# Optimization experiments

Measured on AMD Instinct MI355X. Metric: run time of the kernel, lower is better.

Reference implementation:

```python
import jax, jax.numpy as jnp
import numpy as np
import math

D_MODEL = 512
NHEAD = 8
HEAD = D_MODEL // NHEAD


def _pe(length, d):
    pos = np.arange(length)[:, None].astype(np.float32)
    div = np.exp(np.arange(0, d, 2).astype(np.float32) * (-math.log(10000.0) / d))
    pe = np.zeros((length, d), np.float32)
    pe[:, 0::2] = np.sin(pos * div)
    pe[:, 1::2] = np.cos(pos * div)
    return jnp.asarray(pe)


def _ln(x, g, b, eps=1e-5):
    m = x.mean(-1, keepdims=True)
    v = ((x - m) ** 2).mean(-1, keepdims=True)
    return (x - m) / jnp.sqrt(v + eps) * g + b


def _mha(q_in, k_in, v_in, w_in, b_in, w_out, b_out, mask=None):
    d = q_in.shape[-1]
    wq, wk, wv = jnp.split(w_in, 3, axis=0)
    bq, bk, bv = jnp.split(b_in, 3, axis=0)
    B, Sq, _ = q_in.shape
    Sk = k_in.shape[1]
    q = (q_in @ wq.T + bq).reshape(B, Sq, NHEAD, HEAD)
    k = (k_in @ wk.T + bk).reshape(B, Sk, NHEAD, HEAD)
    v = (v_in @ wv.T + bv).reshape(B, Sk, NHEAD, HEAD)
    s = jnp.einsum('bqhd,bkhd->bhqk', q, k) / math.sqrt(HEAD)
    if mask is not None:
        s = s + mask
    a = jax.nn.softmax(s, axis=-1)
    o = jnp.einsum('bhqk,bkhd->bqhd', a, v).reshape(B, Sq, d)
    return o @ w_out.T + b_out


def setup_inputs() -> dict:
    rng = np.random.default_rng(0)
    def r(*s):
        return jnp.asarray(rng.standard_normal(s, dtype=np.float32) * 0.02)
    L, d, ff, di, do = 6, 512, 2048, 64, 64
    B, S, T = 4, 512, 256
    return dict(
        src=jnp.asarray(rng.standard_normal((B, S, di), dtype=np.float32)),
        tgt=jnp.asarray(rng.standard_normal((B, T, do), dtype=np.float32)),
        enc_in_w=r(d, di), enc_in_b=r(d),
        dec_in_w=r(d, do), dec_in_b=r(d),
        out_w=r(do, d), out_b=r(do),
        enc_attn_w=r(L, 3 * d, d), enc_attn_b=r(L, 3 * d),
        enc_out_w=r(L, d, d), enc_out_b=r(L, d),
        enc_ff1_w=r(L, ff, d), enc_ff1_b=r(L, ff),
        enc_ff2_w=r(L, d, ff), enc_ff2_b=r(L, d),
        enc_ln1_g=jnp.ones((L, d)), enc_ln1_b=jnp.zeros((L, d)),
        enc_ln2_g=jnp.ones((L, d)), enc_ln2_b=jnp.zeros((L, d)),
        dec_sa_w=r(L, 3 * d, d), dec_sa_b=r(L, 3 * d),
        dec_sa_out_w=r(L, d, d), dec_sa_out_b=r(L, d),
        dec_ca_w=r(L, 3 * d, d), dec_ca_b=r(L, 3 * d),
        dec_ca_out_w=r(L, d, d), dec_ca_out_b=r(L, d),
        dec_ff1_w=r(L, ff, d), dec_ff1_b=r(L, ff),
        dec_ff2_w=r(L, d, ff), dec_ff2_b=r(L, d),
        dec_ln1_g=jnp.ones((L, d)), dec_ln1_b=jnp.zeros((L, d)),
        dec_ln2_g=jnp.ones((L, d)), dec_ln2_b=jnp.zeros((L, d)),
        dec_ln3_g=jnp.ones((L, d)), dec_ln3_b=jnp.zeros((L, d)),
    )


def reference(src, tgt, enc_in_w, enc_in_b, dec_in_w, dec_in_b, out_w, out_b,
              enc_attn_w, enc_attn_b, enc_out_w, enc_out_b,
              enc_ff1_w, enc_ff1_b, enc_ff2_w, enc_ff2_b,
              enc_ln1_g, enc_ln1_b, enc_ln2_g, enc_ln2_b,
              dec_sa_w, dec_sa_b, dec_sa_out_w, dec_sa_out_b,
              dec_ca_w, dec_ca_b, dec_ca_out_w, dec_ca_out_b,
              dec_ff1_w, dec_ff1_b, dec_ff2_w, dec_ff2_b,
              dec_ln1_g, dec_ln1_b, dec_ln2_g, dec_ln2_b, dec_ln3_g, dec_ln3_b):
    d = D_MODEL
    sq = math.sqrt(d)
    S, T = src.shape[1], tgt.shape[1]
    L = enc_attn_w.shape[0]
    # encoder: 'cosine' pos encoding (dropout disabled / eval)
    x = (src @ enc_in_w.T + enc_in_b) * sq + _pe(S, d)[None]
    for i in range(L):
        a = _mha(x, x, x, enc_attn_w[i], enc_attn_b[i], enc_out_w[i], enc_out_b[i])
        x = _ln(x + a, enc_ln1_g[i], enc_ln1_b[i])
        f = jax.nn.relu(x @ enc_ff1_w[i].T + enc_ff1_b[i]) @ enc_ff2_w[i].T + enc_ff2_b[i]
        x = _ln(x + f, enc_ln2_g[i], enc_ln2_b[i])
    memory = x
    # decoder: teacher-forced prefix loop == single causal-masked pass.
    # NOTE: original adds pe[0] to EVERY step (pos_encoder on a length-1 slice).
    y = (tgt @ dec_in_w.T + dec_in_b) * sq + _pe(1, d)[0]
    mask = jnp.where(jnp.tril(jnp.ones((T, T), bool)), 0.0, -1e9).astype(y.dtype)
    for i in range(L):
        a = _mha(y, y, y, dec_sa_w[i], dec_sa_b[i], dec_sa_out_w[i], dec_sa_out_b[i], mask)
        y = _ln(y + a, dec_ln1_g[i], dec_ln1_b[i])
        c = _mha(y, memory, memory, dec_ca_w[i], dec_ca_b[i], dec_ca_out_w[i], dec_ca_out_b[i])
        y = _ln(y + c, dec_ln2_g[i], dec_ln2_b[i])
        f = jax.nn.relu(y @ dec_ff1_w[i].T + dec_ff1_b[i]) @ dec_ff2_w[i].T + dec_ff2_b[i]
        y = _ln(y + f, dec_ln3_g[i], dec_ln3_b[i])
    return y @ out_w.T + out_b
```

## Files before the change

kernel.cpp:

```cpp
#include <hip/hip_runtime.h>
#include <hip/hip_bf16.h>
#include <math.h>

#define BB 4
#define SEQ 512
#define TGT 256
#define DM 512
#define FFD 2048
#define NH 8
#define HD 64
#define NL 6

typedef unsigned short u16;
typedef __attribute__((ext_vector_type(2))) unsigned short us2;
typedef __attribute__((ext_vector_type(4))) float f4;
typedef __attribute__((ext_vector_type(4))) unsigned short us4;
typedef __attribute__((ext_vector_type(8))) unsigned short us8;
typedef __attribute__((ext_vector_type(8))) short s8;

__device__ inline u16 f2b(float f) {
    __hip_bfloat16 h = __float2bfloat16(f);
    return *reinterpret_cast<u16*>(&h);
}
__device__ inline float b2f(u16 u) {
    unsigned int x = ((unsigned int)u) << 16;
    float f;
    __builtin_memcpy(&f, &x, 4);
    return f;
}
__device__ inline us4 cvt4(f4 v) {
    us4 u;
    u.x = f2b(v.x); u.y = f2b(v.y); u.z = f2b(v.z); u.w = f2b(v.w);
    return u;
}

struct CastSegs {
    const float* src[24];
    u16* dst[24];
    int cum[25];
    int nseg;
};

__global__ __launch_bounds__(256) void castseg_k(CastSegs cs)
{
    const int g0 = blockIdx.x << 11;
    int s = 0;
    while (g0 >= cs.cum[s + 1]) s++;
    const f4* __restrict__ sp = (const f4*)cs.src[s];
    us4* __restrict__ dp = (us4*)cs.dst[s];
    const int base = g0 - cs.cum[s] + (int)threadIdx.x;

    f4 v[8];
#pragma unroll
    for (int k = 0; k < 8; k++) v[k] = sp[base + (k << 8)];
#pragma unroll
    for (int k = 0; k < 8; k++) dp[base + (k << 8)] = cvt4(v[k]);
}

__global__ void kvbias_k(const float* __restrict__ dec_ca_b, float* __restrict__ out)
{
    int idx = blockIdx.x * blockDim.x + threadIdx.x;
    if (idx >= NL * 2 * DM) return;
    int layer = idx >> 10, j = idx & 1023;
    out[idx] = dec_ca_b[layer * 3 * DM + DM + j];
}

template <int RELU, int OUTF32, int BM, int PE>
__global__ __launch_bounds__(256) void mgemm_k(
    const u16* __restrict__ A, const u16* __restrict__ W,
    const float* __restrict__ bias, const u16* __restrict__ resid,
    void* __restrict__ Cv, int M, int N, int K, float alpha)
{
    constexpr int MI = BM / 32;
    __shared__ u16 As[2][BM][72];
    __shared__ u16 Bs[2][64][72];
    const int bm = blockIdx.y * BM, bn = blockIdx.x * 64;
    const int tid = threadIdx.x;
    const int wave = tid >> 6, lane = tid & 63;
    const int wr = (wave >> 1) * (BM / 2), wc = (wave & 1) * 32;
    const int lm = lane & 15, quad = lane >> 4;
    const int sbr = tid >> 2, sbc = (tid & 3) * 16;
    const int sar = (BM == 64) ? (tid >> 2) : (tid >> 3);
    const int sac = (BM == 64) ? ((tid & 3) * 16) : ((tid & 7) * 8);

    const u16* Arow = A + (size_t)(bm + sar) * K + sac;
    const u16* Wrow = W + (size_t)(bn + sbr) * K + sbc;

    us8 a0 = *(const us8*)(Arow);
    us8 a1;
    if (BM == 64) a1 = *(const us8*)(Arow + 8);
    us8 b0 = *(const us8*)(Wrow);
    us8 b1 = *(const us8*)(Wrow + 8);

    f4 acc[MI][2];
#pragma unroll
    for (int i = 0; i < MI; i++)
#pragma unroll
        for (int j = 0; j < 2; j++) acc[i][j] = (f4)(0.f);

    const int nk = K >> 6;
    *(us8*)&As[0][sar][sac] = a0;
    if (BM == 64) *(us8*)&As[0][sar][sac + 8] = a1;
    *(us8*)&Bs[0][sbr][sbc] = b0;
    *(us8*)&Bs[0][sbr][sbc + 8] = b1;
    __syncthreads();

    for (int t = 0; t < nk; t++) {
        const int cb = t & 1;
        if (t + 1 < nk) {
            int off = (t + 1) << 6;
            a0 = *(const us8*)(Arow + off);
            if (BM == 64) a1 = *(const us8*)(Arow + off + 8);
            b0 = *(const us8*)(Wrow + off);
            b1 = *(const us8*)(Wrow + off + 8);
        }
#pragma unroll
        for (int ks = 0; ks < 2; ks++) {
            s8 af[MI], bfr[2];
#pragma unroll
            for (int i = 0; i < MI; i++) af[i] = *(const s8*)&As[cb][wr + i * 16 + lm][ks * 32 + quad * 8];
#pragma unroll
            for (int j = 0; j < 2; j++) bfr[j] = *(const s8*)&Bs[cb][wc + j * 16 + lm][ks * 32 + quad * 8];
#pragma unroll
            for (int i = 0; i < MI; i++)
#pragma unroll
                for (int j = 0; j < 2; j++)
                    acc[i][j] = __builtin_amdgcn_mfma_f32_16x16x32_bf16(af[i], bfr[j], acc[i][j], 0, 0, 0);
        }
        if (t + 1 < nk) {
            const int nb = cb ^ 1;
            *(us8*)&As[nb][sar][sac] = a0;
            if (BM == 64) *(us8*)&As[nb][sar][sac + 8] = a1;
            *(us8*)&Bs[nb][sbr][sbc] = b0;
            *(us8*)&Bs[nb][sbr][sbc + 8] = b1;
            __syncthreads();
        }
    }

#pragma unroll
    for (int j = 0; j < 2; j++) {
        int n = bn + wc + j * 16 + lm;
        float bv = bias[n];
        float dv = 0.f;
        if (PE == 1) dv = expf((float)(n & ~1) * (-9.210340371976184f / (float)DM));
#pragma unroll
        for (int i = 0; i < MI; i++) {
#pragma unroll
            for (int r = 0; r < 4; r++) {
                int m = bm + wr + i * 16 + quad * 4 + r;
                float v = (acc[i][j][r] + bv) * alpha;
                if (PE == 1) {
                    float ang = (float)(m & (SEQ - 1)) * dv;
                    v += (n & 1) ? cosf(ang) : sinf(ang);
                }
                if (PE == 2) { if (n & 1) v += 1.f; }
                if (RELU) v = fmaxf(v, 0.f);
                size_t off = (size_t)m * N + n;
                if (resid) v += b2f(resid[off]);
                if (OUTF32) ((float*)Cv)[off] = v;
                else        ((u16*)Cv)[off]  = f2b(v);
            }
        }
    }
}

template <int RELU, int KVMAP>
__global__ __launch_bounds__(256) void mgemm128_k(
    const u16* __restrict__ A, const u16* __restrict__ W,
    const float* __restrict__ bias, u16* __restrict__ C,
    int M, int N, int K)
{
    __shared__ u16 As[2][64][72];
    __shared__ u16 Bs[2][128][72];
    const int bm = blockIdx.y * 64, bn = blockIdx.x * 128;
    const int tid = threadIdx.x;
    const int wave = tid >> 6, lane = tid & 63;
    const int wr = (wave >> 1) * 32, wc = (wave & 1) * 64;
    const int lm = lane & 15, quad = lane >> 4;
    const int sar = tid >> 2, sac = (tid & 3) * 16;
    const int sbr = tid >> 1, sbc = (tid & 1) * 32;

    int brow = bn + sbr;
    if (KVMAP) brow = (brow >> 10) * (3 * DM) + DM + (brow & 1023);

    const u16* Arow = A + (size_t)(bm + sar) * K + sac;
    const u16* Wrow = W + (size_t)brow * K + sbc;

    us8 a0 = *(const us8*)(Arow);
    us8 a1 = *(const us8*)(Arow + 8);
    us8 b0 = *(const us8*)(Wrow);
    us8 b1 = *(const us8*)(Wrow + 8);
    us8 b2 = *(const us8*)(Wrow + 16);
    us8 b3 = *(const us8*)(Wrow + 24);

    f4 acc[2][4];
#pragma unroll
    for (int i = 0; i < 2; i++)
#pragma unroll
        for (int j = 0; j < 4; j++) acc[i][j] = (f4)(0.f);

    const int nk = K >> 6;
    *(us8*)&As[0][sar][sac]     = a0;
    *(us8*)&As[0][sar][sac + 8] = a1;
    *(us8*)&Bs[0][sbr][sbc]      = b0;
    *(us8*)&Bs[0][sbr][sbc + 8]  = b1;
    *(us8*)&Bs[0][sbr][sbc + 16] = b2;
    *(us8*)&Bs[0][sbr][sbc + 24] = b3;
    __syncthreads();

    for (int t = 0; t < nk; t++) {
        const int cb = t & 1;
        if (t + 1 < nk) {
            int off = (t + 1) << 6;
            a0 = *(const us8*)(Arow + off);
            a1 = *(const us8*)(Arow + off + 8);
            b0 = *(const us8*)(Wrow + off);
            b1 = *(const us8*)(Wrow + off + 8);
            b2 = *(const us8*)(Wrow + off + 16);
            b3 = *(const us8*)(Wrow + off + 24);
        }
#pragma unroll
        for (int ks = 0; ks < 2; ks++) {
            s8 af[2], bfr[4];
#pragma unroll
            for (int i = 0; i < 2; i++) af[i] = *(const s8*)&As[cb][wr + i * 16 + lm][ks * 32 + quad * 8];
#pragma unroll
            for (int j = 0; j < 4; j++) bfr[j] = *(const s8*)&Bs[cb][wc + j * 16 + lm][ks * 32 + quad * 8];
#pragma unroll
            for (int i = 0; i < 2; i++)
#pragma unroll
                for (int j = 0; j < 4; j++)
                    acc[i][j] = __builtin_amdgcn_mfma_f32_16x16x32_bf16(af[i], bfr[j], acc[i][j], 0, 0, 0);
        }
        if (t + 1 < nk) {
            const int nb = cb ^ 1;
            *(us8*)&As[nb][sar][sac]     = a0;
            *(us8*)&As[nb][sar][sac + 8] = a1;
            *(us8*)&Bs[nb][sbr][sbc]      = b0;
            *(us8*)&Bs[nb][sbr][sbc + 8]  = b1;
            *(us8*)&Bs[nb][sbr][sbc + 16] = b2;
            *(us8*)&Bs[nb][sbr][sbc + 24] = b3;
            __syncthreads();
        }
    }

#pragma unroll
    for (int j = 0; j < 4; j++) {
        int n = bn + wc + j * 16 + lm;
        float bv = bias[n];
#pragma unroll
        for (int i = 0; i < 2; i++) {
#pragma unroll
            for (int r = 0; r < 4; r++) {
                int m = bm + wr + i * 16 + quad * 4 + r;
                float v = acc[i][j][r] + bv;
                if (RELU) v = fmaxf(v, 0.f);
                C[(size_t)m * N + n] = f2b(v);
            }
        }
    }
}

template <int CAUSAL>
__global__ __launch_bounds__(256) void flash_k(
    const u16* __restrict__ Q, int qs,
    const u16* __restrict__ Kp, int ks,
    const u16* __restrict__ V, int vs,
    u16* __restrict__ O, int Sq, int Sk)
{
    __shared__ u16 Qs[64][72];
    __shared__ u16 Ks[128][72];
    __shared__ u16 Vs[64][136];
    __shared__ u16 Ps[4][16][136];
    const int bm = blockIdx.x * 64;
    const int bh = blockIdx.y, b = bh >> 3, h = bh & 7;
    const int tid = threadIdx.x;
    const int wave = tid >> 6, lane = tid & 63;
    const int lm = lane & 15, quad = lane >> 4;

    const u16* Qb = Q + (size_t)(b * Sq + bm) * qs + h * HD;
    {
        int r = tid >> 2, c = (tid & 3) * 16;
        *(us8*)&Qs[r][c]     = *(const us8*)(Qb + (size_t)r * qs + c);
        *(us8*)&Qs[r][c + 8] = *(const us8*)(Qb + (size_t)r * qs + c + 8);
    }

    float mrow[4], lrow[4];
    f4 o[4];
#pragma unroll
    for (int r = 0; r < 4; r++) { mrow[r] = -1e30f; lrow[r] = 0.f; }
#pragma unroll
    for (int nt = 0; nt < 4; nt++) o[nt] = (f4)(0.f);

    const u16* Kb = Kp + (size_t)(b * Sk) * ks + h * HD;
    const u16* Vb = V + (size_t)(b * Sk) * vs + h * HD;
    int nkt = Sk >> 7;
    if (CAUSAL) { int lim = (bm + 63) / 128 + 1; if (lim < nkt) nkt = lim; }

    const int kr = tid >> 3, kc8 = (tid & 7) * 8;
    const int vr = tid & 127, vh = (tid >> 7) * 32;

    for (int kt = 0; kt < nkt; kt++) {
        const u16* Kt = Kb + ((size_t)kt << 7) * ks;
        const u16* Vt = Vb + ((size_t)kt << 7) * vs;
#pragma unroll
        for (int p = 0; p < 4; p++) {
            int r = p * 32 + kr;
            *(us8*)&Ks[r][kc8] = *(const us8*)(Kt + (size_t)r * ks + kc8);
        }
        {
            us8 vv[4];
#pragma unroll
            for (int j = 0; j < 4; j++)
                vv[j] = *(const us8*)(Vt + (size_t)vr * vs + vh + j * 8);
#pragma unroll
            for (int j = 0; j < 4; j++)
#pragma unroll
                for (int e = 0; e < 8; e++)
                    Vs[vh + j * 8 + e][vr] = vv[j][e];
        }
        __syncthreads();

        f4 sa[8];
#pragma unroll
        for (int nt = 0; nt < 8; nt++) sa[nt] = (f4)(0.f);
#pragma unroll
        for (int ks2 = 0; ks2 < 2; ks2++) {
            s8 aq = *(const s8*)&Qs[wave * 16 + lm][ks2 * 32 + quad * 8];
#pragma unroll
            for (int nt = 0; nt < 8; nt++) {
                s8 bk = *(const s8*)&Ks[nt * 16 + lm][ks2 * 32 + quad * 8];
                sa[nt] = __builtin_amdgcn_mfma_f32_16x16x32_bf16(aq, bk, sa[nt], 0, 0, 0);
            }
        }
        float tmx[4] = {-1e30f, -1e30f, -1e30f, -1e30f};
#pragma unroll
        for (int nt = 0; nt < 8; nt++) {
#pragma unroll
            for (int r = 0; r < 4; r++) {
                float v = sa[nt][r] * 0.125f;
                if (CAUSAL) {
                    int col = (kt << 7) + nt * 16 + lm;
                    int row = bm + wave * 16 + quad * 4 + r;
                    if (col > row) v = -1e30f;
                }
                sa[nt][r] = v;
                tmx[r] = fmaxf(tmx[r], v);
            }
        }
#pragma unroll
        for (int st = 1; st < 16; st <<= 1)
#pragma unroll
            for (int r = 0; r < 4; r++) tmx[r] = fmaxf(tmx[r], __shfl_xor(tmx[r], st));
        float al[4];
#pragma unroll
        for (int r = 0; r < 4; r++) {
            float mn = fmaxf(mrow[r], tmx[r]);
            al[r] = __expf(mrow[r] - mn);
            mrow[r] = mn;
        }
        float ts[4] = {0.f, 0.f, 0.f, 0.f};
#pragma unroll
        for (int nt = 0; nt < 8; nt++) {
#pragma unroll
            for (int r = 0; r < 4; r++) {
                float pe = __expf(sa[nt][r] - mrow[r]);
                sa[nt][r] = pe;
                ts[r] += pe;
            }
        }
#pragma unroll
        for (int st = 1; st < 16; st <<= 1)
#pragma unroll
            for (int r = 0; r < 4; r++) ts[r] += __shfl_xor(ts[r], st);
#pragma unroll
        for (int r = 0; r < 4; r++) lrow[r] = lrow[r] * al[r] + ts[r];
#pragma unroll
        for (int nt = 0; nt < 4; nt++)
#pragma unroll
            for (int r = 0; r < 4; r++) o[nt][r] *= al[r];
#pragma unroll
        for (int nt = 0; nt < 8; nt++)
#pragma unroll
            for (int r = 0; r < 4; r++)
                Ps[wave][quad * 4 + r][nt * 16 + lm] = f2b(sa[nt][r]);
#pragma unroll
        for (int kc = 0; kc < 4; kc++) {
            s8 ap = *(const s8*)&Ps[wave][lm][kc * 32 + quad * 8];
#pragma unroll
            for (int nt = 0; nt < 4; nt++) {
                s8 bv = *(const s8*)&Vs[nt * 16 + lm][kc * 32 + quad * 8];
                o[nt] = __builtin_amdgcn_mfma_f32_16x16x32_bf16(ap, bv, o[nt], 0, 0, 0);
            }
        }
        __syncthreads();
    }

    float inv[4];
#pragma unroll
    for (int r = 0; r < 4; r++) inv[r] = 1.f / lrow[r];
#pragma unroll
    for (int nt = 0; nt < 4; nt++) {
#pragma unroll
        for (int r = 0; r < 4; r++) {
            int m = bm + wave * 16 + quad * 4 + r;
            O[(size_t)(b * Sq + m) * DM + h * HD + nt * 16 + lm] = f2b(o[nt][r] * inv[r]);
        }
    }
}

__global__ __launch_bounds__(256) void ln_k(u16* __restrict__ x,
                                            const float* __restrict__ g,
                                            const float* __restrict__ b)
{
    const int wave = threadIdx.x >> 6, lane = threadIdx.x & 63;
    const int row = blockIdx.x * 4 + wave;
    u16* xr = x + (size_t)row * DM + lane * 8;
    us8 v8 = *(const us8*)xr;
    float v[8];
    float s = 0.f;
#pragma unroll
    for (int e = 0; e < 8; e++) { v[e] = b2f(v8[e]); s += v[e]; }
#pragma unroll
    for (int st = 1; st < 64; st <<= 1) s += __shfl_xor(s, st);
    float mean = s * (1.f / DM);
    float q = 0.f;
#pragma unroll
    for (int e = 0; e < 8; e++) { float d = v[e] - mean; q += d * d; }
#pragma unroll
    for (int st = 1; st < 64; st <<= 1) q += __shfl_xor(q, st);
    float rstd = rsqrtf(q * (1.f / DM) + 1e-5f);
    f4 g0 = *(const f4*)(g + lane * 8), g1 = *(const f4*)(g + lane * 8 + 4);
    f4 b0 = *(const f4*)(b + lane * 8), b1 = *(const f4*)(b + lane * 8 + 4);
    us8 o;
#pragma unroll
    for (int e = 0; e < 4; e++) {
        o[e]     = f2b((v[e]     - mean) * rstd * g0[e] + b0[e]);
        o[e + 4] = f2b((v[e + 4] - mean) * rstd * g1[e] + b1[e]);
    }
    *(us8*)xr = o;
}

static inline dim3 mg64(int M, int N) { return dim3(N / 64, M / 64); }
static inline dim3 mg32(int M, int N) { return dim3(N / 64, M / 32); }
static inline dim3 mg128(int M, int N) { return dim3(N / 128, M / 64); }

extern "C" void kernel_launch(void* const* d_in, const int* in_sizes, int n_in,
                              void* d_out, int out_size, void* d_ws, size_t ws_size,
                              hipStream_t stream)
{
    const float* src       = (const float*)d_in[0];
    const float* tgt       = (const float*)d_in[1];
    const float* enc_in_w  = (const float*)d_in[2];
    const float* enc_in_b  = (const float*)d_in[3];
    const float* dec_in_w  = (const float*)d_in[4];
    const float* dec_in_b  = (const float*)d_in[5];
    const float* out_w     = (const float*)d_in[6];
    const float* out_b     = (const float*)d_in[7];
    const float* enc_attn_w = (const float*)d_in[8];
    const float* enc_attn_b = (const float*)d_in[9];
    const float* enc_out_w  = (const float*)d_in[10];
    const float* enc_out_b  = (const float*)d_in[11];
    const float* enc_ff1_w  = (const float*)d_in[12];
    const float* enc_ff1_b  = (const float*)d_in[13];
    const float* enc_ff2_w  = (const float*)d_in[14];
    const float* enc_ff2_b  = (const float*)d_in[15];
    const float* enc_ln1_g  = (const float*)d_in[16];
    const float* enc_ln1_b  = (const float*)d_in[17];
    const float* enc_ln2_g  = (const float*)d_in[18];
    const float* enc_ln2_b  = (const float*)d_in[19];
    const float* dec_sa_w     = (const float*)d_in[20];
    const float* dec_sa_b     = (const float*)d_in[21];
    const float* dec_sa_out_w = (const float*)d_in[22];
    const float* dec_sa_out_b = (const float*)d_in[23];
    const float* dec_ca_w     = (const float*)d_in[24];
    const float* dec_ca_b     = (const float*)d_in[25];
    const float* dec_ca_out_w = (const float*)d_in[26];
    const float* dec_ca_out_b = (const float*)d_in[27];
    const float* dec_ff1_w    = (const float*)d_in[28];
    const float* dec_ff1_b    = (const float*)d_in[29];
    const float* dec_ff2_w    = (const float*)d_in[30];
    const float* dec_ff2_b    = (const float*)d_in[31];
    const float* dec_ln1_g    = (const float*)d_in[32];
    const float* dec_ln1_b    = (const float*)d_in[33];
    const float* dec_ln2_g    = (const float*)d_in[34];
    const float* dec_ln2_b    = (const float*)d_in[35];
    const float* dec_ln3_g    = (const float*)d_in[36];
    const float* dec_ln3_b    = (const float*)d_in[37];

    const int ME = BB * SEQ;
    const int MD = BB * TGT;
    const int BH = BB * NH;
    const float SQD = 22.627416997969522f;

    const size_t SZ_ATTN = (size_t)NL * 3 * DM * DM;
    const size_t SZ_OUT  = (size_t)NL * DM * DM;
    const size_t SZ_FF   = (size_t)NL * FFD * DM;

    float* fp = (float*)d_ws;
    float* kvbias = fp; fp += NL * 2 * DM;
    u16* p = (u16*)fp;
    u16* xa   = p; p += (size_t)ME * DM;
    u16* xb   = p; p += (size_t)ME * DM;
    u16* reg1 = p; p += (size_t)ME * FFD;
    u16* tbuf = p; p += (size_t)ME * DM;
    u16* ya   = p; p += (size_t)MD * DM;
    u16* yb   = p; p += (size_t)MD * DM;
    u16* kvall = p; p += (size_t)ME * NL * 2 * DM;
    u16* src_b     = p; p += (size_t)ME * HD;
    u16* tgt_b     = p; p += (size_t)MD * HD;
    u16* enc_in_wb = p; p += (size_t)DM * HD;
    u16* dec_in_wb = p; p += (size_t)DM * HD;
    u16* out_wb    = p; p += (size_t)HD * DM;
    u16* enc_at_wb = p; p += SZ_ATTN;
    u16* enc_ow_wb = p; p += SZ_OUT;
    u16* enc_f1_wb = p; p += SZ_FF;
    u16* enc_f2_wb = p; p += SZ_FF;
    u16* dec_sa_wb = p; p += SZ_ATTN;
    u16* dec_sao_wb = p; p += SZ_OUT;
    u16* dec_ca_wb = p; p += SZ_ATTN;
    u16* dec_cao_wb = p; p += SZ_OUT;
    u16* dec_f1_wb = p; p += SZ_FF;
    u16* dec_f2_wb = p; p += SZ_FF;

    CastSegs cs;
    int ns = 0;
    auto seg = [&](const float* s, u16* d, size_t n) {
        cs.src[ns] = s; cs.dst[ns] = d;
        cs.cum[ns + 1] = cs.cum[ns] + (int)(n / 4);
        ns++;
    };
    cs.cum[0] = 0;
    seg(src,          src_b,     (size_t)ME * HD);
    seg(tgt,          tgt_b,     (size_t)MD * HD);
    seg(enc_in_w,     enc_in_wb, (size_t)DM * HD);
    seg(dec_in_w,     dec_in_wb, (size_t)DM * HD);
    seg(out_w,        out_wb,    (size_t)HD * DM);
    seg(enc_attn_w,   enc_at_wb, SZ_ATTN);
    seg(enc_out_w,    enc_ow_wb, SZ_OUT);
    seg(enc_ff1_w,    enc_f1_wb, SZ_FF);
    seg(enc_ff2_w,    enc_f2_wb, SZ_FF);
    seg(dec_sa_w,     dec_sa_wb, SZ_ATTN);
    seg(dec_sa_out_w, dec_sao_wb, SZ_OUT);
    seg(dec_ca_w,     dec_ca_wb, SZ_ATTN);
    seg(dec_ca_out_w, dec_cao_wb, SZ_OUT);
    seg(dec_ff1_w,    dec_f1_wb, SZ_FF);
    seg(dec_ff2_w,    dec_f2_wb, SZ_FF);
    cs.nseg = ns;
    castseg_k<<<cs.cum[ns] >> 11, 256, 0, stream>>>(cs);
    kvbias_k<<<(NL * 2 * DM + 255) / 256, 256, 0, stream>>>(dec_ca_b, kvbias);

    mgemm_k<0, 0, 64, 1><<<mg64(ME, DM), 256, 0, stream>>>(src_b, enc_in_wb, enc_in_b, nullptr, xa, ME, DM, HD, SQD);

    u16* cur = xa; u16* alt = xb;
    for (int i = 0; i < NL; i++) {
        const u16* W = enc_at_wb + (size_t)i * 3 * DM * DM;
        const float* Bw = enc_attn_b + (size_t)i * 3 * DM;
        mgemm128_k<0, 0><<<mg128(ME, 3 * DM), 256, 0, stream>>>(cur, W, Bw, reg1, ME, 3 * DM, DM);
        flash_k<0><<<dim3(SEQ / 64, BH), 256, 0, stream>>>(reg1, 3 * DM, reg1 + DM, 3 * DM, reg1 + 2 * DM, 3 * DM, tbuf, SEQ, SEQ);
        mgemm_k<0, 0, 32, 0><<<mg32(ME, DM), 256, 0, stream>>>(tbuf, enc_ow_wb + (size_t)i * DM * DM, enc_out_b + (size_t)i * DM, cur, alt, ME, DM, DM, 1.f);
        ln_k<<<ME / 4, 256, 0, stream>>>(alt, enc_ln1_g + (size_t)i * DM, enc_ln1_b + (size_t)i * DM);
        { u16* t = cur; cur = alt; alt = t; }
        mgemm128_k<1, 0><<<mg128(ME, FFD), 256, 0, stream>>>(cur, enc_f1_wb + (size_t)i * FFD * DM, enc_ff1_b + (size_t)i * FFD, reg1, ME, FFD, DM);
        mgemm_k<0, 0, 32, 0><<<mg32(ME, DM), 256, 0, stream>>>(reg1, enc_f2_wb + (size_t)i * DM * FFD, enc_ff2_b + (size_t)i * DM, cur, alt, ME, DM, FFD, 1.f);
        ln_k<<<ME / 4, 256, 0, stream>>>(alt, enc_ln2_g + (size_t)i * DM, enc_ln2_b + (size_t)i * DM);
        { u16* t = cur; cur = alt; alt = t; }
    }
    u16* mem = cur;

    mgemm128_k<0, 1><<<mg128(ME, NL * 2 * DM), 256, 0, stream>>>(mem, dec_ca_wb, kvbias, kvall, ME, NL * 2 * DM, DM);

    mgemm_k<0, 0, 32, 2><<<mg32(MD, DM), 256, 0, stream>>>(tgt_b, dec_in_wb, dec_in_b, nullptr, ya, MD, DM, HD, SQD);

    u16* dc = ya; u16* da = yb;
    for (int i = 0; i < NL; i++) {
        const u16* W = dec_sa_wb + (size_t)i * 3 * DM * DM;
        const float* Bw = dec_sa_b + (size_t)i * 3 * DM;
        mgemm128_k<0, 0><<<mg128(MD, 3 * DM), 256, 0, stream>>>(dc, W, Bw, reg1, MD, 3 * DM, DM);
        flash_k<1><<<dim3(TGT / 64, BH), 256, 0, stream>>>(reg1, 3 * DM, reg1 + DM, 3 * DM, reg1 + 2 * DM, 3 * DM, tbuf, TGT, TGT);
        mgemm_k<0, 0, 32, 0><<<mg32(MD, DM), 256, 0, stream>>>(tbuf, dec_sao_wb + (size_t)i * DM * DM, dec_sa_out_b + (size_t)i * DM, dc, da, MD, DM, DM, 1.f);
        ln_k<<<MD / 4, 256, 0, stream>>>(da, dec_ln1_g + (size_t)i * DM, dec_ln1_b + (size_t)i * DM);
        { u16* t = dc; dc = da; da = t; }

        const u16* Wc = dec_ca_wb + (size_t)i * 3 * DM * DM;
        const float* Bc = dec_ca_b + (size_t)i * 3 * DM;
        u16* qbuf = reg1;
        mgemm_k<0, 0, 32, 0><<<mg32(MD, DM), 256, 0, stream>>>(dc, Wc, Bc, nullptr, qbuf, MD, DM, DM, 1.f);
        const u16* kvl = kvall + (size_t)i * 2 * DM;
        flash_k<0><<<dim3(TGT / 64, BH), 256, 0, stream>>>(qbuf, DM, kvl, NL * 2 * DM, kvl + DM, NL * 2 * DM, tbuf, TGT, SEQ);
        mgemm_k<0, 0, 32, 0><<<mg32(MD, DM), 256, 0, stream>>>(tbuf, dec_cao_wb + (size_t)i * DM * DM, dec_ca_out_b + (size_t)i * DM, dc, da, MD, DM, DM, 1.f);
        ln_k<<<MD / 4, 256, 0, stream>>>(da, dec_ln2_g + (size_t)i * DM, dec_ln2_b + (size_t)i * DM);
        { u16* t = dc; dc = da; da = t; }

        mgemm128_k<1, 0><<<mg128(MD, FFD), 256, 0, stream>>>(dc, dec_f1_wb + (size_t)i * FFD * DM, dec_ff1_b + (size_t)i * FFD, reg1, MD, FFD, DM);
        mgemm_k<0, 0, 32, 0><<<mg32(MD, DM), 256, 0, stream>>>(reg1, dec_f2_wb + (size_t)i * DM * FFD, dec_ff2_b + (size_t)i * DM, dc, da, MD, DM, FFD, 1.f);
        ln_k<<<MD / 4, 256, 0, stream>>>(da, dec_ln3_g + (size_t)i * DM, dec_ln3_b + (size_t)i * DM);
        { u16* t = dc; dc = da; da = t; }
    }

    mgemm_k<0, 1, 32, 0><<<mg32(MD, HD), 256, 0, stream>>>(dc, out_wb, out_b, nullptr, (float*)d_out, MD, HD, DM, 1.f);
}
```

Measured before the change: 1.273 ms.

## Drop upfront weight cast; load fp32 weights and convert inside GEMM tile loads

Removes the large upfront fp32-to-bf16 conversion pass over all layer weights. The GEMM kernels instead read fp32 weights directly and convert them while staging tiles into shared memory. This avoids a separate full write and reread of the weights, at the cost of twice the global bytes per weight tile inside each GEMM plus the conversion work there. The flash kernel's V transpose load also changes from vectorized row reads to scalar per-element loads.

```diff
diff --git a/kernel.cpp b/kernel.cpp
--- a/kernel.cpp
+++ b/kernel.cpp
@@ -12,7 +12,6 @@
 #define NL 6
 
 typedef unsigned short u16;
-typedef __attribute__((ext_vector_type(2))) unsigned short us2;
 typedef __attribute__((ext_vector_type(4))) float f4;
 typedef __attribute__((ext_vector_type(4))) unsigned short us4;
 typedef __attribute__((ext_vector_type(8))) unsigned short us8;
@@ -34,10 +33,30 @@
     return u;
 }
 
+template <int WF32> struct wvec {};
+template <> struct wvec<0> { us8 v; };
+template <> struct wvec<1> { f4 lo, hi; };
+
+__device__ inline void wload(wvec<0>& d, const void* W, size_t idx) {
+    d.v = *(const us8*)((const u16*)W + idx);
+}
+__device__ inline void wload(wvec<1>& d, const void* W, size_t idx) {
+    const float* p = (const float*)W + idx;
+    d.lo = *(const f4*)p; d.hi = *(const f4*)(p + 4);
+}
+__device__ inline us8 wcvt(const wvec<0>& d) { return d.v; }
+__device__ inline us8 wcvt(const wvec<1>& d) {
+    us4 l = cvt4(d.lo), h = cvt4(d.hi);
+    us8 o;
+#pragma unroll
+    for (int e = 0; e < 4; e++) { o[e] = l[e]; o[e + 4] = h[e]; }
+    return o;
+}
+
 struct CastSegs {
-    const float* src[24];
-    u16* dst[24];
-    int cum[25];
+    const float* src[8];
+    u16* dst[8];
+    int cum[9];
     int nseg;
 };
 
@@ -65,9 +84,9 @@
     out[idx] = dec_ca_b[layer * 3 * DM + DM + j];
 }
 
-template <int RELU, int OUTF32, int BM, int PE>
+template <int RELU, int OUTF32, int BM, int PE, int WF32>
 __global__ __launch_bounds__(256) void mgemm_k(
-    const u16* __restrict__ A, const u16* __restrict__ W,
+    const u16* __restrict__ A, const void* __restrict__ W,
     const float* __restrict__ bias, const u16* __restrict__ resid,
     void* __restrict__ Cv, int M, int N, int K, float alpha)
 {
@@ -84,13 +103,14 @@
     const int sac = (BM == 64) ? ((tid & 3) * 16) : ((tid & 7) * 8);
 
     const u16* Arow = A + (size_t)(bm + sar) * K + sac;
-    const u16* Wrow = W + (size_t)(bn + sbr) * K + sbc;
+    const size_t wb0 = (size_t)(bn + sbr) * K + sbc;
 
     us8 a0 = *(const us8*)(Arow);
     us8 a1;
     if (BM == 64) a1 = *(const us8*)(Arow + 8);
-    us8 b0 = *(const us8*)(Wrow);
-    us8 b1 = *(const us8*)(Wrow + 8);
+    wvec<WF32> b0, b1;
+    wload(b0, W, wb0);
+    wload(b1, W, wb0 + 8);
 
     f4 acc[MI][2];
 #pragma unroll
@@ -101,8 +121,8 @@
     const int nk = K >> 6;
     *(us8*)&As[0][sar][sac] = a0;
     if (BM == 64) *(us8*)&As[0][sar][sac + 8] = a1;
-    *(us8*)&Bs[0][sbr][sbc] = b0;
-    *(us8*)&Bs[0][sbr][sbc + 8] = b1;
+    *(us8*)&Bs[0][sbr][sbc] = wcvt(b0);
+    *(us8*)&Bs[0][sbr][sbc + 8] = wcvt(b1);
     __syncthreads();
 
     for (int t = 0; t < nk; t++) {
@@ -111,8 +131,8 @@
             int off = (t + 1) << 6;
             a0 = *(const us8*)(Arow + off);
             if (BM == 64) a1 = *(const us8*)(Arow + off + 8);
-            b0 = *(const us8*)(Wrow + off);
-            b1 = *(const us8*)(Wrow + off + 8);
+            wload(b0, W, wb0 + off);
+            wload(b1, W, wb0 + off + 8);
         }
 #pragma unroll
         for (int ks = 0; ks < 2; ks++) {
@@ -131,8 +151,8 @@
             const int nb = cb ^ 1;
             *(us8*)&As[nb][sar][sac] = a0;
             if (BM == 64) *(us8*)&As[nb][sar][sac + 8] = a1;
-            *(us8*)&Bs[nb][sbr][sbc] = b0;
-            *(us8*)&Bs[nb][sbr][sbc + 8] = b1;
+            *(us8*)&Bs[nb][sbr][sbc] = wcvt(b0);
+            *(us8*)&Bs[nb][sbr][sbc + 8] = wcvt(b1);
             __syncthreads();
         }
     }
@@ -164,9 +184,9 @@
     }
 }
 
-template <int RELU, int KVMAP>
+template <int RELU, int KVMAP, int WF32>
 __global__ __launch_bounds__(256) void mgemm128_k(
-    const u16* __restrict__ A, const u16* __restrict__ W,
+    const u16* __restrict__ A, const void* __restrict__ W,
     const float* __restrict__ bias, u16* __restrict__ C,
     int M, int N, int K)
 {
@@ -184,14 +204,15 @@
     if (KVMAP) brow = (brow >> 10) * (3 * DM) + DM + (brow & 1023);
 
     const u16* Arow = A + (size_t)(bm + sar) * K + sac;
-    const u16* Wrow = W + (size_t)brow * K + sbc;
+    const size_t wb0 = (size_t)brow * K + sbc;
 
     us8 a0 = *(const us8*)(Arow);
     us8 a1 = *(const us8*)(Arow + 8);
-    us8 b0 = *(const us8*)(Wrow);
-    us8 b1 = *(const us8*)(Wrow + 8);
-    us8 b2 = *(const us8*)(Wrow + 16);
-    us8 b3 = *(const us8*)(Wrow + 24);
+    wvec<WF32> b0, b1, b2, b3;
+    wload(b0, W, wb0);
+    wload(b1, W, wb0 + 8);
+    wload(b2, W, wb0 + 16);
+    wload(b3, W, wb0 + 24);
 
     f4 acc[2][4];
 #pragma unroll
@@ -202,10 +223,10 @@
     const int nk = K >> 6;
     *(us8*)&As[0][sar][sac]     = a0;
     *(us8*)&As[0][sar][sac + 8] = a1;
-    *(us8*)&Bs[0][sbr][sbc]      = b0;
-    *(us8*)&Bs[0][sbr][sbc + 8]  = b1;
-    *(us8*)&Bs[0][sbr][sbc + 16] = b2;
-    *(us8*)&Bs[0][sbr][sbc + 24] = b3;
+    *(us8*)&Bs[0][sbr][sbc]      = wcvt(b0);
+    *(us8*)&Bs[0][sbr][sbc + 8]  = wcvt(b1);
+    *(us8*)&Bs[0][sbr][sbc + 16] = wcvt(b2);
+    *(us8*)&Bs[0][sbr][sbc + 24] = wcvt(b3);
     __syncthreads();
 
     for (int t = 0; t < nk; t++) {
@@ -214,10 +235,10 @@
             int off = (t + 1) << 6;
             a0 = *(const us8*)(Arow + off);
             a1 = *(const us8*)(Arow + off + 8);
-            b0 = *(const us8*)(Wrow + off);
-            b1 = *(const us8*)(Wrow + off + 8);
-            b2 = *(const us8*)(Wrow + off + 16);
-            b3 = *(const us8*)(Wrow + off + 24);
+            wload(b0, W, wb0 + off);
+            wload(b1, W, wb0 + off + 8);
+            wload(b2, W, wb0 + off + 16);
+            wload(b3, W, wb0 + off + 24);
         }
 #pragma unroll
         for (int ks = 0; ks < 2; ks++) {
@@ -236,10 +257,10 @@
             const int nb = cb ^ 1;
             *(us8*)&As[nb][sar][sac]     = a0;
             *(us8*)&As[nb][sar][sac + 8] = a1;
-            *(us8*)&Bs[nb][sbr][sbc]      = b0;
-            *(us8*)&Bs[nb][sbr][sbc + 8]  = b1;
-            *(us8*)&Bs[nb][sbr][sbc + 16] = b2;
-            *(us8*)&Bs[nb][sbr][sbc + 24] = b3;
+            *(us8*)&Bs[nb][sbr][sbc]      = wcvt(b0);
+            *(us8*)&Bs[nb][sbr][sbc + 8]  = wcvt(b1);
+            *(us8*)&Bs[nb][sbr][sbc + 16] = wcvt(b2);
+            *(us8*)&Bs[nb][sbr][sbc + 24] = wcvt(b3);
             __syncthreads();
         }
     }
@@ -297,8 +318,8 @@
     int nkt = Sk >> 7;
     if (CAUSAL) { int lim = (bm + 63) / 128 + 1; if (lim < nkt) nkt = lim; }
 
+    const int vd = tid & 63, vkb = tid >> 6;
     const int kr = tid >> 3, kc8 = (tid & 7) * 8;
-    const int vr = tid & 127, vh = (tid >> 7) * 32;
 
     for (int kt = 0; kt < nkt; kt++) {
         const u16* Kt = Kb + ((size_t)kt << 7) * ks;
@@ -308,16 +329,10 @@
             int r = p * 32 + kr;
             *(us8*)&Ks[r][kc8] = *(const us8*)(Kt + (size_t)r * ks + kc8);
         }
-        {
-            us8 vv[4];
-#pragma unroll
-            for (int j = 0; j < 4; j++)
-                vv[j] = *(const us8*)(Vt + (size_t)vr * vs + vh + j * 8);
-#pragma unroll
-            for (int j = 0; j < 4; j++)
-#pragma unroll
-                for (int e = 0; e < 8; e++)
-                    Vs[vh + j * 8 + e][vr] = vv[j][e];
+#pragma unroll
+        for (int p = 0; p < 32; p++) {
+            int kv = p * 4 + vkb;
+            Vs[vd][kv] = Vt[(size_t)kv * vs + vd];
         }
         __syncthreads();
 
@@ -493,10 +508,6 @@
     const int BH = BB * NH;
     const float SQD = 22.627416997969522f;
 
-    const size_t SZ_ATTN = (size_t)NL * 3 * DM * DM;
-    const size_t SZ_OUT  = (size_t)NL * DM * DM;
-    const size_t SZ_FF   = (size_t)NL * FFD * DM;
-
     float* fp = (float*)d_ws;
     float* kvbias = fp; fp += NL * 2 * DM;
     u16* p = (u16*)fp;
@@ -512,16 +523,6 @@
     u16* enc_in_wb = p; p += (size_t)DM * HD;
     u16* dec_in_wb = p; p += (size_t)DM * HD;
     u16* out_wb    = p; p += (size_t)HD * DM;
-    u16* enc_at_wb = p; p += SZ_ATTN;
-    u16* enc_ow_wb = p; p += SZ_OUT;
-    u16* enc_f1_wb = p; p += SZ_FF;
-    u16* enc_f2_wb = p; p += SZ_FF;
-    u16* dec_sa_wb = p; p += SZ_ATTN;
-    u16* dec_sao_wb = p; p += SZ_OUT;
-    u16* dec_ca_wb = p; p += SZ_ATTN;
-    u16* dec_cao_wb = p; p += SZ_OUT;
-    u16* dec_f1_wb = p; p += SZ_FF;
-    u16* dec_f2_wb = p; p += SZ_FF;
 
     CastSegs cs;
     int ns = 0;
@@ -531,72 +532,56 @@
         ns++;
     };
     cs.cum[0] = 0;
-    seg(src,          src_b,     (size_t)ME * HD);
-    seg(tgt,          tgt_b,     (size_t)MD * HD);
-    seg(enc_in_w,     enc_in_wb, (size_t)DM * HD);
-    seg(dec_in_w,     dec_in_wb, (size_t)DM * HD);
-    seg(out_w,        out_wb,    (size_t)HD * DM);
-    seg(enc_attn_w,   enc_at_wb, SZ_ATTN);
-    seg(enc_out_w,    enc_ow_wb, SZ_OUT);
-    seg(enc_ff1_w,    enc_f1_wb, SZ_FF);
-    seg(enc_ff2_w,    enc_f2_wb, SZ_FF);
-    seg(dec_sa_w,     dec_sa_wb, SZ_ATTN);
-    seg(dec_sa_out_w, dec_sao_wb, SZ_OUT);
-    seg(dec_ca_w,     dec_ca_wb, SZ_ATTN);
-    seg(dec_ca_out_w, dec_cao_wb, SZ_OUT);
-    seg(dec_ff1_w,    dec_f1_wb, SZ_FF);
-    seg(dec_ff2_w,    dec_f2_wb, SZ_FF);
+    seg(src,      src_b,     (size_t)ME * HD);
+    seg(tgt,      tgt_b,     (size_t)MD * HD);
+    seg(enc_in_w, enc_in_wb, (size_t)DM * HD);
+    seg(dec_in_w, dec_in_wb, (size_t)DM * HD);
+    seg(out_w,    out_wb,    (size_t)HD * DM);
     cs.nseg = ns;
     castseg_k<<<cs.cum[ns] >> 11, 256, 0, stream>>>(cs);
     kvbias_k<<<(NL * 2 * DM + 255) / 256, 256, 0, stream>>>(dec_ca_b, kvbias);
 
-    mgemm_k<0, 0, 64, 1><<<mg64(ME, DM), 256, 0, stream>>>(src_b, enc_in_wb, enc_in_b, nullptr, xa, ME, DM, HD, SQD);
+    mgemm_k<0, 0, 64, 1, 0><<<mg64(ME, DM), 256, 0, stream>>>(src_b, enc_in_wb, enc_in_b, nullptr, xa, ME, DM, HD, SQD);
 
     u16* cur = xa; u16* alt = xb;
     for (int i = 0; i < NL; i++) {
-        const u16* W = enc_at_wb + (size_t)i * 3 * DM * DM;
-        const float* Bw = enc_attn_b + (size_t)i * 3 * DM;
-        mgemm128_k<0, 0><<<mg128(ME, 3 * DM), 256, 0, stream>>>(cur, W, Bw, reg1, ME, 3 * DM, DM);
+        mgemm128_k<0, 0, 1><<<mg128(ME, 3 * DM), 256, 0, stream>>>(cur, enc_attn_w + (size_t)i * 3 * DM * DM, enc_attn_b + (size_t)i * 3 * DM, reg1, ME, 3 * DM, DM);
         flash_k<0><<<dim3(SEQ / 64, BH), 256, 0, stream>>>(reg1, 3 * DM, reg1 + DM, 3 * DM, reg1 + 2 * DM, 3 * DM, tbuf, SEQ, SEQ);
-        mgemm_k<0, 0, 32, 0><<<mg32(ME, DM), 256, 0, stream>>>(tbuf, enc_ow_wb + (size_t)i * DM * DM, enc_out_b + (size_t)i * DM, cur, alt, ME, DM, DM, 1.f);
+        mgemm_k<0, 0, 32, 0, 1><<<mg32(ME, DM), 256, 0, stream>>>(tbuf, enc_out_w + (size_t)i * DM * DM, enc_out_b + (size_t)i * DM, cur, alt, ME, DM, DM, 1.f);
         ln_k<<<ME / 4, 256, 0, stream>>>(alt, enc_ln1_g + (size_t)i * DM, enc_ln1_b + (size_t)i * DM);
         { u16* t = cur; cur = alt; alt = t; }
-        mgemm128_k<1, 0><<<mg128(ME, FFD), 256, 0, stream>>>(cur, enc_f1_wb + (size_t)i * FFD * DM, enc_ff1_b + (size_t)i * FFD, reg1, ME, FFD, DM);
-        mgemm_k<0, 0, 32, 0><<<mg32(ME, DM), 256, 0, stream>>>(reg1, enc_f2_wb + (size_t)i * DM * FFD, enc_ff2_b + (size_t)i * DM, cur, alt, ME, DM, FFD, 1.f);
+        mgemm128_k<1, 0, 1><<<mg128(ME, FFD), 256, 0, stream>>>(cur, enc_ff1_w + (size_t)i * FFD * DM, enc_ff1_b + (size_t)i * FFD, reg1, ME, FFD, DM);
+        mgemm_k<0, 0, 32, 0, 1><<<mg32(ME, DM), 256, 0, stream>>>(reg1, enc_ff2_w + (size_t)i * DM * FFD, enc_ff2_b + (size_t)i * DM, cur, alt, ME, DM, FFD, 1.f);
         ln_k<<<ME / 4, 256, 0, stream>>>(alt, enc_ln2_g + (size_t)i * DM, enc_ln2_b + (size_t)i * DM);
         { u16* t = cur; cur = alt; alt = t; }
     }
     u16* mem = cur;
 
-    mgemm128_k<0, 1><<<mg128(ME, NL * 2 * DM), 256, 0, stream>>>(mem, dec_ca_wb, kvbias, kvall, ME, NL * 2 * DM, DM);
-
-    mgemm_k<0, 0, 32, 2><<<mg32(MD, DM), 256, 0, stream>>>(tgt_b, dec_in_wb, dec_in_b, nullptr, ya, MD, DM, HD, SQD);
+    mgemm128_k<0, 1, 1><<<mg128(ME, NL * 2 * DM), 256, 0, stream>>>(mem, dec_ca_w, kvbias, kvall, ME, NL * 2 * DM, DM);
+
+    mgemm_k<0, 0, 32, 2, 0><<<mg32(MD, DM), 256, 0, stream>>>(tgt_b, dec_in_wb, dec_in_b, nullptr, ya, MD, DM, HD, SQD);
 
     u16* dc = ya; u16* da = yb;
     for (int i = 0; i < NL; i++) {
-        const u16* W = dec_sa_wb + (size_t)i * 3 * DM * DM;
-        const float* Bw = dec_sa_b + (size_t)i * 3 * DM;
-        mgemm128_k<0, 0><<<mg128(MD, 3 * DM), 256, 0, stream>>>(dc, W, Bw, reg1, MD, 3 * DM, DM);
+        mgemm128_k<0, 0, 1><<<mg128(MD, 3 * DM), 256, 0, stream>>>(dc, dec_sa_w + (size_t)i * 3 * DM * DM, dec_sa_b + (size_t)i * 3 * DM, reg1, MD, 3 * DM, DM);
         flash_k<1><<<dim3(TGT / 64, BH), 256, 0, stream>>>(reg1, 3 * DM, reg1 + DM, 3 * DM, reg1 + 2 * DM, 3 * DM, tbuf, TGT, TGT);
-        mgemm_k<0, 0, 32, 0><<<mg32(MD, DM), 256, 0, stream>>>(tbuf, dec_sao_wb + (size_t)i * DM * DM, dec_sa_out_b + (size_t)i * DM, dc, da, MD, DM, DM, 1.f);
+        mgemm_k<0, 0, 32, 0, 1><<<mg32(MD, DM), 256, 0, stream>>>(tbuf, dec_sa_out_w + (size_t)i * DM * DM, dec_sa_out_b + (size_t)i * DM, dc, da, MD, DM, DM, 1.f);
         ln_k<<<MD / 4, 256, 0, stream>>>(da, dec_ln1_g + (size_t)i * DM, dec_ln1_b + (size_t)i * DM);
         { u16* t = dc; dc = da; da = t; }
 
-        const u16* Wc = dec_ca_wb + (size_t)i * 3 * DM * DM;
-        const float* Bc = dec_ca_b + (size_t)i * 3 * DM;
         u16* qbuf = reg1;
-        mgemm_k<0, 0, 32, 0><<<mg32(MD, DM), 256, 0, stream>>>(dc, Wc, Bc, nullptr, qbuf, MD, DM, DM, 1.f);
+        mgemm_k<0, 0, 32, 0, 1><<<mg32(MD, DM), 256, 0, stream>>>(dc, dec_ca_w + (size_t)i * 3 * DM * DM, dec_ca_b + (size_t)i * 3 * DM, nullptr, qbuf, MD, DM, DM, 1.f);
         const u16* kvl = kvall + (size_t)i * 2 * DM;
         flash_k<0><<<dim3(TGT / 64, BH), 256, 0, stream>>>(qbuf, DM, kvl, NL * 2 * DM, kvl + DM, NL * 2 * DM, tbuf, TGT, SEQ);
-        mgemm_k<0, 0, 32, 0><<<mg32(MD, DM), 256, 0, stream>>>(tbuf, dec_cao_wb + (size_t)i * DM * DM, dec_ca_out_b + (size_t)i * DM, dc, da, MD, DM, DM, 1.f);
+        mgemm_k<0, 0, 32, 0, 1><<<mg32(MD, DM), 256, 0, stream>>>(tbuf, dec_ca_out_w + (size_t)i * DM * DM, dec_ca_out_b + (size_t)i * DM, dc, da, MD, DM, DM, 1.f);
         ln_k<<<MD / 4, 256, 0, stream>>>(da, dec_ln2_g + (size_t)i * DM, dec_ln2_b + (size_t)i * DM);
         { u16* t = dc; dc = da; da = t; }
 
-        mgemm128_k<1, 0><<<mg128(MD, FFD), 256, 0, stream>>>(dc, dec_f1_wb + (size_t)i * FFD * DM, dec_ff1_b + (size_t)i * FFD, reg1, MD, FFD, DM);
-        mgemm_k<0, 0, 32, 0><<<mg32(MD, DM), 256, 0, stream>>>(reg1, dec_f2_wb + (size_t)i * DM * FFD, dec_ff2_b + (size_t)i * DM, dc, da, MD, DM, FFD, 1.f);
+        mgemm128_k<1, 0, 1><<<mg128(MD, FFD), 256, 0, stream>>>(dc, dec_ff1_w + (size_t)i * FFD * DM, dec_ff1_b + (size_t)i * FFD, reg1, MD, FFD, DM);
+        mgemm_k<0, 0, 32, 0, 1><<<mg32(MD, DM), 256, 0, stream>>>(reg1, dec_ff2_w + (size_t)i * DM * FFD, dec_ff2_b + (size_t)i * DM, dc, da, MD, DM, FFD, 1.f);
         ln_k<<<MD / 4, 256, 0, stream>>>(da, dec_ln3_g + (size_t)i * DM, dec_ln3_b + (size_t)i * DM);
         { u16* t = dc; dc = da; da = t; }
     }
 
-    mgemm_k<0, 1, 32, 0><<<mg32(MD, HD), 256, 0, stream>>>(dc, out_wb, out_b, nullptr, (float*)d_out, MD, HD, DM, 1.f);
-}
+    mgemm_k<0, 1, 32, 0, 0><<<mg32(MD, HD), 256, 0, stream>>>(dc, out_wb, out_b, nullptr, (float*)d_out, MD, HD, DM, 1.f);
+}
```

Result: slower. 1.659 ms (+30.3%).
